# Performance work log

Measured on AMD Instinct MI355X. Metric: run time of the kernel, lower is better.

The kernel has to match this reference:

```python
import jax, jax.numpy as jnp
import numpy as np

V, C, T, H, L, B = 32000, 1024, 1024, 16, 8, 4
HS = C // H
STD = 0.02


def _layernorm(x, g, b, eps=1e-5):
    m = jnp.mean(x, axis=-1, keepdims=True)
    v = jnp.mean(jnp.square(x - m), axis=-1, keepdims=True)
    return (x - m) * jax.lax.rsqrt(v + eps) * g + b


def setup_inputs() -> dict:
    key = jax.random.key(0)
    ks = jax.random.split(key, 16)
    n = lambda k, shape: (jax.random.normal(k, shape, dtype=jnp.float32) * STD)
    return {
        "index": jax.random.randint(ks[0], (B, T), 0, V),
        "targets": jax.random.randint(ks[1], (B, T), 0, V),
        "tok_emb": n(ks[2], (V, C)),
        "pos_emb": n(ks[3], (T, C)),
        "wq": n(ks[4], (L, C, C)),
        "wk": n(ks[5], (L, C, C)),
        "wv": n(ks[6], (L, C, C)),
        "wo": n(ks[7], (L, C, C)),
        "bo": jnp.zeros((L, C), jnp.float32),
        "w1": n(ks[8], (L, C, 4 * C)),
        "b1": jnp.zeros((L, 4 * C), jnp.float32),
        "w2": n(ks[9], (L, 4 * C, C)),
        "b2": jnp.zeros((L, C), jnp.float32),
        "ln1_g": jnp.ones((L, C), jnp.float32),
        "ln1_b": jnp.zeros((L, C), jnp.float32),
        "ln2_g": jnp.ones((L, C), jnp.float32),
        "ln2_b": jnp.zeros((L, C), jnp.float32),
        "lnf_g": jnp.ones((C,), jnp.float32),
        "lnf_b": jnp.zeros((C,), jnp.float32),
        "lm_w": n(ks[10], (C, V)),
        "lm_b": jnp.zeros((V,), jnp.float32),
    }


def reference(index, targets, tok_emb, pos_emb, wq, wk, wv, wo, bo, w1, b1, w2,
              b2, ln1_g, ln1_b, ln2_g, ln2_b, lnf_g, lnf_b, lm_w, lm_b):
    b, t = index.shape
    x = tok_emb[index] + pos_emb[:t]                      # [B,T,C]
    causal = jnp.tril(jnp.ones((t, t), dtype=bool))       # tril mask
    scale = HS ** -0.5
    for l in range(L):  # fixed small layer loop
        q = (x @ wq[l]).reshape(b, t, H, HS)
        k = (x @ wk[l]).reshape(b, t, H, HS)
        v = (x @ wv[l]).reshape(b, t, H, HS)
        scores = jnp.einsum('bqhd,bkhd->bhqk', q, k) * scale
        scores = jnp.where(causal, scores, -jnp.inf)
        w = jax.nn.softmax(scores, axis=-1)               # dropout p=0 -> identity
        att = jnp.einsum('bhqk,bkhd->bqhd', w, v).reshape(b, t, C)
        x = _layernorm(x + att @ wo[l] + bo[l], ln1_g[l], ln1_b[l])
        h = jax.nn.relu(x @ w1[l] + b1[l])
        x = _layernorm(x + h @ w2[l] + b2[l], ln2_g[l], ln2_b[l])
    x = _layernorm(x, lnf_g, lnf_b)
    logits = (x @ lm_w + lm_b).reshape(b * t, V)
    logp = jax.nn.log_softmax(logits, axis=-1)
    loss = -jnp.take_along_axis(logp, targets.reshape(-1, 1), axis=1).mean()
    return logits, loss
```

## Files before the change

### kernel.cpp

```cpp
#include <hip/hip_runtime.h>

typedef unsigned short u16;
typedef __attribute__((ext_vector_type(4))) float f32x4;
typedef __attribute__((ext_vector_type(8))) short s16x8;

static constexpr int V = 32000;
static constexpr int C = 1024;
static constexpr int T = 1024;
static constexpr int H = 16;
static constexpr int L = 8;
static constexpr int B = 4;
static constexpr int HS = 64;
static constexpr int BT = B * T;
static constexpr int C4 = 4 * C;
static constexpr int C3 = 3 * C;

__device__ __forceinline__ u16 f2bf(float f) {
  union { float f; unsigned u; } v; v.f = f;
  unsigned r = v.u + 0x7fffu + ((v.u >> 16) & 1u);
  return (u16)(r >> 16);
}

__device__ __forceinline__ void gload16(const u16* g, u16* l) {
  __builtin_amdgcn_global_load_lds(
      (const __attribute__((address_space(1))) void*)g,
      (__attribute__((address_space(3))) void*)l, 16, 0, 0);
}

__device__ __forceinline__ float blockReduceSum(float v) {
  __shared__ float red[4];
  int lane = threadIdx.x & 63, w = threadIdx.x >> 6;
#pragma unroll
  for (int m = 32; m >= 1; m >>= 1) v += __shfl_xor(v, m, 64);
  if (lane == 0) red[w] = v;
  __syncthreads();
  float r = red[0] + red[1] + red[2] + red[3];
  __syncthreads();
  return r;
}

__global__ __launch_bounds__(256) void k_embed(
    const int* __restrict__ idx, const float* __restrict__ tok,
    const float* __restrict__ pos, float* __restrict__ x, u16* __restrict__ xb) {
  int bt = blockIdx.x;
  int t = bt & (T - 1);
  int row = idx[bt];
  const float* te = tok + (size_t)row * C;
  const float* pe = pos + (size_t)t * C;
  float* xo = x + (size_t)bt * C;
  u16* xbo = xb + (size_t)bt * C;
  for (int c = threadIdx.x; c < C; c += 256) {
    float v = te[c] + pe[c];
    xo[c] = v;
    xbo[c] = f2bf(v);
  }
}

__global__ __launch_bounds__(256) void k_transpose(
    const float* __restrict__ W, u16* __restrict__ Wt, int K, int N,
    size_t sW, size_t sWt) {
  __shared__ float tile[64][65];
  const float* Wz = W + sW * blockIdx.z;
  u16* Wtz = Wt + sWt * blockIdx.z;
  int n0 = blockIdx.x * 64, k0 = blockIdx.y * 64;
  int tc = threadIdx.x & 63, tr = threadIdx.x >> 6;
#pragma unroll
  for (int i = 0; i < 16; ++i) {
    int r = tr + i * 4;
    tile[r][tc] = Wz[(size_t)(k0 + r) * N + (n0 + tc)];
  }
  __syncthreads();
#pragma unroll
  for (int i = 0; i < 16; ++i) {
    int r = tr + i * 4;
    Wtz[(size_t)(n0 + r) * K + (k0 + tc)] = f2bf(tile[tc][r]);
  }
}

__global__ __launch_bounds__(256) void k_vtrans(
    const u16* __restrict__ qkv, u16* __restrict__ vt) {
  __shared__ u16 tile[64][72];
  int bid = blockIdx.x;
  int tc = bid & 15, h = (bid >> 4) & 15, b = bid >> 8;
  int t0 = tc * 64;
  const size_t base = (size_t)b * T * C3 + 2 * C + (size_t)h * HS;
  int tid = threadIdx.x;
  int r = tid >> 3, c8 = (tid & 7) * 8;
#pragma unroll
  for (int it = 0; it < 2; ++it) {
    int row = r + it * 32;
    *(s16x8*)&tile[row][c8] =
        *(const s16x8*)&qkv[base + (size_t)(t0 + row) * C3 + c8];
  }
  __syncthreads();
  const size_t vbase = (size_t)(b * H + h) * HS * T + t0;
#pragma unroll
  for (int it = 0; it < 2; ++it) {
    int d = (tid >> 3) + it * 32;
    s16x8 o;
#pragma unroll
    for (int j = 0; j < 8; ++j) o[j] = (short)tile[c8 + j][d];
    *(s16x8*)&vt[vbase + (size_t)d * T + c8] = o;
  }
}

template <int OUT_BF16, int RELU, int HAS_BIAS, int HAS_RES>
__global__ __launch_bounds__(256, 2) void k_gemm(
    const u16* __restrict__ A, const u16* __restrict__ Bt,
    const float* __restrict__ bias, const float* __restrict__ Res,
    float* __restrict__ Cf, u16* __restrict__ Cb, int M, int N, int K) {
  __shared__ u16 As[128 * 32];
  __shared__ u16 Bs[128 * 32];
  int tid = threadIdx.x;
  int lane = tid & 63, wid = tid >> 6;
  int lm = lane & 15, lg = lane >> 4;
  int wm = wid >> 1, wn = wid & 1;

  unsigned nbx = gridDim.x;
  unsigned nwg = nbx * gridDim.y;
  unsigned orig = blockIdx.y * nbx + blockIdx.x;
  unsigned f = ((nwg & 7u) == 0u) ? (orig & 7u) * (nwg >> 3) + (orig >> 3) : orig;
  int mb = (int)(f / nbx) * 128, nb = (int)(f % nbx) * 128;

  f32x4 acc[4][4];
#pragma unroll
  for (int i = 0; i < 4; ++i)
#pragma unroll
    for (int j = 0; j < 4; ++j) acc[i][j] = f32x4{0.f, 0.f, 0.f, 0.f};

  int r0 = tid >> 2, q0 = tid & 3;
  int r1 = (256 + tid) >> 2, q1 = tid & 3;
  const u16* a0 = A + (size_t)(mb + r0) * K + q0 * 8;
  const u16* a1 = A + (size_t)(mb + r1) * K + q1 * 8;
  const u16* b0 = Bt + (size_t)(nb + r0) * K + q0 * 8;
  const u16* b1 = Bt + (size_t)(nb + r1) * K + q1 * 8;
  u16* lA0 = &As[wid * 512];
  u16* lA1 = &As[2048 + wid * 512];
  u16* lB0 = &Bs[wid * 512];
  u16* lB1 = &Bs[2048 + wid * 512];

  int nK = K >> 5;
  for (int kb = 0; kb < nK; ++kb) {
    __syncthreads();
    int ko = kb * 32;
    gload16(a0 + ko, lA0);
    gload16(a1 + ko, lA1);
    gload16(b0 + ko, lB0);
    gload16(b1 + ko, lB1);
    __syncthreads();
    s16x8 af[4], bfr[4];
#pragma unroll
    for (int m = 0; m < 4; ++m)
      af[m] = *(const s16x8*)&As[(wm * 64 + m * 16 + lm) * 32 + lg * 8];
#pragma unroll
    for (int n = 0; n < 4; ++n)
      bfr[n] = *(const s16x8*)&Bs[(wn * 64 + n * 16 + lm) * 32 + lg * 8];
#pragma unroll
    for (int m = 0; m < 4; ++m)
#pragma unroll
      for (int n = 0; n < 4; ++n)
        acc[m][n] = __builtin_amdgcn_mfma_f32_16x16x32_bf16(af[m], bfr[n],
                                                            acc[m][n], 0, 0, 0);
  }
#pragma unroll
  for (int m = 0; m < 4; ++m) {
#pragma unroll
    for (int n = 0; n < 4; ++n) {
      int col = nb + wn * 64 + n * 16 + lm;
      float bv = HAS_BIAS ? bias[col] : 0.0f;
#pragma unroll
      for (int r = 0; r < 4; ++r) {
        int row = mb + wm * 64 + m * 16 + lg * 4 + r;
        float v = acc[m][n][r] + bv;
        if (HAS_RES) v += Res[(size_t)row * N + col];
        if (RELU) v = v > 0.f ? v : 0.f;
        if (OUT_BF16)
          Cb[(size_t)row * N + col] = f2bf(v);
        else
          Cf[(size_t)row * N + col] = v;
      }
    }
  }
}

template <int OUT_BF16, int RELU, int HAS_BIAS, int HAS_RES>
__global__ __launch_bounds__(512) void k_gemm256(
    const u16* __restrict__ A, const u16* __restrict__ Bt,
    const float* __restrict__ bias, const float* __restrict__ Res,
    float* __restrict__ Cf, u16* __restrict__ Cb, int M, int N, int K) {
  __shared__ u16 As[2][16384];
  __shared__ u16 Bs[2][16384];
  const int tid = threadIdx.x;
  const int lane = tid & 63, wid = tid >> 6;
  const int lm = lane & 15, lg = lane >> 4;
  const int wr = wid >> 2, wc = wid & 3;

  unsigned nbx = gridDim.x;
  unsigned nwg = nbx * gridDim.y;
  unsigned orig = blockIdx.y * nbx + blockIdx.x;
  unsigned f = ((nwg & 7u) == 0u) ? (orig & 7u) * (nwg >> 3) + (orig >> 3) : orig;
  const int mb = (int)(f / nbx) * 256, nb = (int)(f % nbx) * 256;

  int aoff[4], boff[4], ldso[4];
#pragma unroll
  for (int h = 0; h < 4; ++h) {
    const int kk = h >> 1, p = h & 1;
    int rem = p * 512 + tid;
    int rblk = rem >> 6;
    int rem2 = rem & 63;
    int row16 = rem2 >> 2, psl = rem2 & 3;
    int sl = psl ^ ((row16 >> 1) & 3);
    int grow = rblk * 16 + row16;
    int gk = kk * 32 + sl * 8;
    aoff[h] = (mb + grow) * K + gk;
    boff[h] = (nb + grow) * K + gk;
    ldso[h] = kk * 8192 + p * 4096 + wid * 512;
  }
  const int lo = lm * 32 + ((lg ^ ((lm >> 1) & 3)) << 3);

  f32x4 acc[8][4];
#pragma unroll
  for (int i = 0; i < 8; ++i)
#pragma unroll
    for (int j = 0; j < 4; ++j) acc[i][j] = f32x4{0.f, 0.f, 0.f, 0.f};

  const int nK = K >> 6;
  gload16(A + aoff[0], &As[0][ldso[0]]);
  gload16(A + aoff[1], &As[0][ldso[1]]);
  gload16(Bt + boff[0], &Bs[0][ldso[0]]);
  gload16(Bt + boff[1], &Bs[0][ldso[1]]);
  gload16(A + aoff[2], &As[0][ldso[2]]);
  gload16(A + aoff[3], &As[0][ldso[3]]);
  gload16(Bt + boff[2], &Bs[0][ldso[2]]);
  gload16(Bt + boff[3], &Bs[0][ldso[3]]);
  asm volatile("s_waitcnt vmcnt(4)" ::: "memory");
  __builtin_amdgcn_s_barrier();

  for (int t = 0; t < nK; ++t) {
    const int buf = t & 1, nbuf = buf ^ 1;
    const bool pre = (t + 1 < nK);
    const int nk64 = (t + 1) * 64;
    s16x8 af[4], bfr[4];
#pragma unroll
    for (int m = 0; m < 4; ++m)
      af[m] = *(const s16x8*)&As[buf][(wr * 8 + m) * 512 + lo];
#pragma unroll
    for (int n = 0; n < 4; ++n)
      bfr[n] = *(const s16x8*)&Bs[buf][(wc * 4 + n) * 512 + lo];
    if (pre) {
      gload16(A + aoff[0] + nk64, &As[nbuf][ldso[0]]);
      gload16(A + aoff[1] + nk64, &As[nbuf][ldso[1]]);
    }
    __builtin_amdgcn_s_barrier();
    __builtin_amdgcn_s_setprio(1);
#pragma unroll
    for (int m = 0; m < 4; ++m)
#pragma unroll
      for (int n = 0; n < 4; ++n)
        acc[m][n] = __builtin_amdgcn_mfma_f32_16x16x32_bf16(af[m], bfr[n],
                                                            acc[m][n], 0, 0, 0);
    __builtin_amdgcn_s_setprio(0);
    __builtin_amdgcn_s_barrier();
#pragma unroll
    for (int m = 0; m < 4; ++m)
      af[m] = *(const s16x8*)&As[buf][(wr * 8 + 4 + m) * 512 + lo];
    if (pre) {
      gload16(Bt + boff[0] + nk64, &Bs[nbuf][ldso[0]]);
      gload16(Bt + boff[1] + nk64, &Bs[nbuf][ldso[1]]);
    }
    __builtin_amdgcn_s_barrier();
    __builtin_amdgcn_s_setprio(1);
#pragma unroll
    for (int m = 0; m < 4; ++m)
#pragma unroll
      for (int n = 0; n < 4; ++n)
        acc[m + 4][n] = __builtin_amdgcn_mfma_f32_16x16x32_bf16(
            af[m], bfr[n], acc[m + 4][n], 0, 0, 0);
    __builtin_amdgcn_s_setprio(0);
    __builtin_amdgcn_s_barrier();
#pragma unroll
    for (int m = 0; m < 4; ++m)
      af[m] = *(const s16x8*)&As[buf][8192 + (wr * 8 + m) * 512 + lo];
#pragma unroll
    for (int n = 0; n < 4; ++n)
      bfr[n] = *(const s16x8*)&Bs[buf][8192 + (wc * 4 + n) * 512 + lo];
    if (pre) {
      gload16(A + aoff[2] + nk64, &As[nbuf][ldso[2]]);
      gload16(A + aoff[3] + nk64, &As[nbuf][ldso[3]]);
      asm volatile("s_waitcnt vmcnt(6)" ::: "memory");
    } else {
      asm volatile("s_waitcnt vmcnt(0)" ::: "memory");
    }
    __builtin_amdgcn_s_barrier();
    __builtin_amdgcn_s_setprio(1);
#pragma unroll
    for (int m = 0; m < 4; ++m)
#pragma unroll
      for (int n = 0; n < 4; ++n)
        acc[m][n] = __builtin_amdgcn_mfma_f32_16x16x32_bf16(af[m], bfr[n],
                                                            acc[m][n], 0, 0, 0);
    __builtin_amdgcn_s_setprio(0);
    __builtin_amdgcn_s_barrier();
#pragma unroll
    for (int m = 0; m < 4; ++m)
      af[m] = *(const s16x8*)&As[buf][8192 + (wr * 8 + 4 + m) * 512 + lo];
    if (pre) {
      gload16(Bt + boff[2] + nk64, &Bs[nbuf][ldso[2]]);
      gload16(Bt + boff[3] + nk64, &Bs[nbuf][ldso[3]]);
      asm volatile("s_waitcnt vmcnt(4)" ::: "memory");
    }
    __builtin_amdgcn_s_barrier();
    __builtin_amdgcn_s_setprio(1);
#pragma unroll
    for (int m = 0; m < 4; ++m)
#pragma unroll
      for (int n = 0; n < 4; ++n)
        acc[m + 4][n] = __builtin_amdgcn_mfma_f32_16x16x32_bf16(
            af[m], bfr[n], acc[m + 4][n], 0, 0, 0);
    __builtin_amdgcn_s_setprio(0);
    __builtin_amdgcn_s_barrier();
  }
  float bv[4];
#pragma unroll
  for (int n = 0; n < 4; ++n)
    bv[n] = HAS_BIAS ? bias[nb + wc * 64 + n * 16 + lm] : 0.0f;
#pragma unroll
  for (int m = 0; m < 8; ++m) {
#pragma unroll
    for (int r = 0; r < 4; ++r) {
      int row = mb + wr * 128 + m * 16 + lg * 4 + r;
#pragma unroll
      for (int n = 0; n < 4; ++n) {
        int col = nb + wc * 64 + n * 16 + lm;
        float v = acc[m][n][r] + bv[n];
        if (HAS_RES) v += Res[(size_t)row * N + col];
        if (RELU) v = v > 0.f ? v : 0.f;
        if (OUT_BF16)
          Cb[(size_t)row * N + col] = f2bf(v);
        else
          Cf[(size_t)row * N + col] = v;
      }
    }
  }
}

__global__ __launch_bounds__(256) void k_attn(
    const u16* __restrict__ qkv, const u16* __restrict__ vt,
    u16* __restrict__ o) {
  constexpr int PP = 72;
  __shared__ u16 Ks[64 * 64];
  __shared__ u16 Vs[64 * 64];
  __shared__ u16 Ps[4][16 * PP];
  int bid = blockIdx.x;
  int qt = bid & 15, h = (bid >> 4) & 15, b = bid >> 8;
  int tid = threadIdx.x, lane = tid & 63, wid = tid >> 6;
  int lm = lane & 15, lg = lane >> 4;
  const size_t rowbase = (size_t)b * T * C3 + (size_t)h * HS;
  const u16* kbase = qkv + rowbase + C;
  const u16* vbase = vt + (size_t)(b * H + h) * HS * T;
  int qb = qt * 64;
  int qw = qb + wid * 16;
  const float scale = 0.125f;

  s16x8 qf[2];
#pragma unroll
  for (int s = 0; s < 2; ++s)
    qf[s] = *(const s16x8*)&qkv[rowbase + (size_t)(qw + lm) * C3 + s * 32 + lg * 8];

  float m_[4], l_[4];
  f32x4 oacc[4];
#pragma unroll
  for (int r = 0; r < 4; ++r) { m_[r] = -3e38f; l_[r] = 0.f; }
#pragma unroll
  for (int n = 0; n < 4; ++n) oacc[n] = f32x4{0.f, 0.f, 0.f, 0.f};

  const int sr = tid >> 3, scs = (tid & 7) ^ (sr & 7);
  const int swz0 = ((lg) ^ (lm & 7)) * 8;
  const int swz1 = ((4 + lg) ^ (lm & 7)) * 8;

  for (int kt = 0; kt <= qt; ++kt) {
    __syncthreads();
    gload16(kbase + (size_t)(kt * 64 + sr) * C3 + scs * 8, &Ks[wid * 512]);
    gload16(kbase + (size_t)(kt * 64 + sr + 32) * C3 + scs * 8,
            &Ks[2048 + wid * 512]);
    gload16(vbase + (size_t)sr * T + kt * 64 + scs * 8, &Vs[wid * 512]);
    gload16(vbase + (size_t)(sr + 32) * T + kt * 64 + scs * 8,
            &Vs[2048 + wid * 512]);
    __syncthreads();

    f32x4 s[4];
#pragma unroll
    for (int ch = 0; ch < 4; ++ch) s[ch] = f32x4{0.f, 0.f, 0.f, 0.f};
#pragma unroll
    for (int ch = 0; ch < 4; ++ch) {
      s16x8 k0 = *(const s16x8*)&Ks[(ch * 16 + lm) * 64 + swz0];
      s16x8 k1 = *(const s16x8*)&Ks[(ch * 16 + lm) * 64 + swz1];
      s[ch] = __builtin_amdgcn_mfma_f32_16x16x32_bf16(qf[0], k0, s[ch], 0, 0, 0);
      s[ch] = __builtin_amdgcn_mfma_f32_16x16x32_bf16(qf[1], k1, s[ch], 0, 0, 0);
    }
    if (kt == qt) {
#pragma unroll
      for (int ch = 0; ch < 4; ++ch) {
        int col = kt * 64 + ch * 16 + lm;
#pragma unroll
        for (int r = 0; r < 4; ++r) {
          int row = qw + lg * 4 + r;
          s[ch][r] = (col <= row) ? s[ch][r] * scale : -3e38f;
        }
      }
    } else {
#pragma unroll
      for (int ch = 0; ch < 4; ++ch)
#pragma unroll
        for (int r = 0; r < 4; ++r) s[ch][r] *= scale;
    }
    float rmax[4];
#pragma unroll
    for (int r = 0; r < 4; ++r)
      rmax[r] = fmaxf(fmaxf(s[0][r], s[1][r]), fmaxf(s[2][r], s[3][r]));
#pragma unroll
    for (int mm = 1; mm < 16; mm <<= 1)
#pragma unroll
      for (int r = 0; r < 4; ++r)
        rmax[r] = fmaxf(rmax[r], __shfl_xor(rmax[r], mm, 16));
    float alpha[4], rsum[4];
#pragma unroll
    for (int r = 0; r < 4; ++r) {
      float mn = fmaxf(m_[r], rmax[r]);
      alpha[r] = __expf(m_[r] - mn);
      m_[r] = mn;
      rsum[r] = 0.f;
    }
#pragma unroll
    for (int ch = 0; ch < 4; ++ch)
#pragma unroll
      for (int r = 0; r < 4; ++r) {
        float e = __expf(s[ch][r] - m_[r]);
        s[ch][r] = e;
        rsum[r] += e;
      }
#pragma unroll
    for (int mm = 1; mm < 16; mm <<= 1)
#pragma unroll
      for (int r = 0; r < 4; ++r) rsum[r] += __shfl_xor(rsum[r], mm, 16);
#pragma unroll
    for (int r = 0; r < 4; ++r) l_[r] = l_[r] * alpha[r] + rsum[r];
#pragma unroll
    for (int n = 0; n < 4; ++n)
#pragma unroll
      for (int r = 0; r < 4; ++r) oacc[n][r] *= alpha[r];
#pragma unroll
    for (int r = 0; r < 4; ++r) {
      int pr = lg * 4 + r;
#pragma unroll
      for (int ch = 0; ch < 4; ++ch)
        Ps[wid][pr * PP + ch * 16 + lm] = f2bf(s[ch][r]);
    }
    s16x8 pa0 = *(const s16x8*)&Ps[wid][lm * PP + lg * 8];
    s16x8 pa1 = *(const s16x8*)&Ps[wid][lm * PP + 32 + lg * 8];
#pragma unroll
    for (int n = 0; n < 4; ++n) {
      s16x8 v0 = *(const s16x8*)&Vs[(n * 16 + lm) * 64 + swz0];
      s16x8 v1 = *(const s16x8*)&Vs[(n * 16 + lm) * 64 + swz1];
      oacc[n] = __builtin_amdgcn_mfma_f32_16x16x32_bf16(pa0, v0, oacc[n], 0, 0, 0);
      oacc[n] = __builtin_amdgcn_mfma_f32_16x16x32_bf16(pa1, v1, oacc[n], 0, 0, 0);
    }
  }
  const size_t obase = (size_t)b * T * C + (size_t)h * HS;
  float inv[4];
#pragma unroll
  for (int r = 0; r < 4; ++r) inv[r] = 1.0f / l_[r];
#pragma unroll
  for (int n = 0; n < 4; ++n)
#pragma unroll
    for (int r = 0; r < 4; ++r)
      o[obase + (size_t)(qw + lg * 4 + r) * C + n * 16 + lm] =
          f2bf(oacc[n][r] * inv[r]);
}

__global__ __launch_bounds__(256) void k_ln(
    const float* __restrict__ in, const float* __restrict__ g,
    const float* __restrict__ bsh, float* __restrict__ xout,
    u16* __restrict__ xbout) {
  int row = blockIdx.x;
  const float* xr = in + (size_t)row * C;
  int tid = threadIdx.x;
  float vals[4];
  float s = 0.f;
#pragma unroll
  for (int i = 0; i < 4; ++i) {
    float vv = xr[tid + i * 256];
    vals[i] = vv;
    s += vv;
  }
  s = blockReduceSum(s);
  float mean = s * (1.0f / C);
  float s2 = 0.f;
#pragma unroll
  for (int i = 0; i < 4; ++i) {
    float d = vals[i] - mean;
    s2 += d * d;
  }
  s2 = blockReduceSum(s2);
  float rstd = rsqrtf(s2 * (1.0f / C) + 1e-5f);
#pragma unroll
  for (int i = 0; i < 4; ++i) {
    int c = tid + i * 256;
    float y = (vals[i] - mean) * rstd * g[c] + bsh[c];
    xout[(size_t)row * C + c] = y;
    xbout[(size_t)row * C + c] = f2bf(y);
  }
}

__global__ __launch_bounds__(256) void k_rowloss(
    const float* __restrict__ logits, const int* __restrict__ tgt,
    float* __restrict__ rowloss) {
  int row = blockIdx.x;
  const float* lr = logits + (size_t)row * V;
  const f32x4* lr4 = (const f32x4*)lr;
  int tid = threadIdx.x;
  float m = -3e38f, s = 0.f;
  for (int i = tid; i < V / 4; i += 256) {
    f32x4 v = lr4[i];
#pragma unroll
    for (int j = 0; j < 4; ++j) {
      float x = v[j];
      if (x > m) {
        s = s * __expf(m - x) + 1.f;
        m = x;
      } else {
        s += __expf(x - m);
      }
    }
  }
#pragma unroll
  for (int d = 1; d < 64; d <<= 1) {
    float mo = __shfl_xor(m, d, 64), so = __shfl_xor(s, d, 64);
    float mn = fmaxf(m, mo);
    s = s * __expf(m - mn) + so * __expf(mo - mn);
    m = mn;
  }
  __shared__ float sm[4], ss[4];
  int w = tid >> 6;
  if ((tid & 63) == 0) { sm[w] = m; ss[w] = s; }
  __syncthreads();
  if (tid == 0) {
    float M = fmaxf(fmaxf(sm[0], sm[1]), fmaxf(sm[2], sm[3]));
    float S = ss[0] * __expf(sm[0] - M) + ss[1] * __expf(sm[1] - M) +
              ss[2] * __expf(sm[2] - M) + ss[3] * __expf(sm[3] - M);
    rowloss[row] = (M + logf(S)) - lr[tgt[row]];
  }
}

__global__ __launch_bounds__(256) void k_lossreduce(
    const float* __restrict__ rowloss, float* __restrict__ out) {
  __shared__ float red[256];
  int tid = threadIdx.x;
  float s = 0.f;
  for (int i = tid; i < BT; i += 256) s += rowloss[i];
  red[tid] = s;
  __syncthreads();
  for (int m = 128; m >= 1; m >>= 1) {
    if (tid < m) red[tid] += red[tid + m];
    __syncthreads();
  }
  if (tid == 0) out[0] = red[0] * (1.0f / BT);
}

extern "C" void kernel_launch(void* const* d_in, const int* in_sizes, int n_in,
                              void* d_out, int out_size, void* d_ws,
                              size_t ws_size, hipStream_t stream) {
  (void)in_sizes; (void)n_in; (void)out_size; (void)ws_size;
  const int* index = (const int*)d_in[0];
  const int* targets = (const int*)d_in[1];
  const float* tok_emb = (const float*)d_in[2];
  const float* pos_emb = (const float*)d_in[3];
  const float* wq = (const float*)d_in[4];
  const float* wk = (const float*)d_in[5];
  const float* wv = (const float*)d_in[6];
  const float* wo = (const float*)d_in[7];
  const float* bo = (const float*)d_in[8];
  const float* w1 = (const float*)d_in[9];
  const float* b1 = (const float*)d_in[10];
  const float* w2 = (const float*)d_in[11];
  const float* b2 = (const float*)d_in[12];
  const float* ln1_g = (const float*)d_in[13];
  const float* ln1_b = (const float*)d_in[14];
  const float* ln2_g = (const float*)d_in[15];
  const float* ln2_b = (const float*)d_in[16];
  const float* lnf_g = (const float*)d_in[17];
  const float* lnf_b = (const float*)d_in[18];
  const float* lm_w = (const float*)d_in[19];
  const float* lm_b = (const float*)d_in[20];

  float* logits = (float*)d_out;
  float* loss = logits + (size_t)BT * V;

  size_t off = 0;
  auto alloc = [&](size_t bytes) -> void* {
    off = (off + 255) & ~(size_t)255;
    void* p = (void*)((char*)d_ws + off);
    off += bytes;
    return p;
  };
  u16* wqkv_t = (u16*)alloc((size_t)L * C3 * C * 2);
  u16* wo_t = (u16*)alloc((size_t)L * C * C * 2);
  u16* w1_t = (u16*)alloc((size_t)L * C * C4 * 2);
  u16* w2_t = (u16*)alloc((size_t)L * C4 * C * 2);
  u16* lmw_t = (u16*)alloc((size_t)V * C * 2);
  float* x = (float*)alloc((size_t)BT * C * 4);
  float* tmp = (float*)alloc((size_t)BT * C * 4);
  u16* xb = (u16*)alloc((size_t)BT * C * 2);
  u16* qkvb = (u16*)alloc((size_t)BT * C3 * 2);
  u16* vtb = (u16*)alloc((size_t)BT * C * 2);
  u16* attb = (u16*)alloc((size_t)BT * C * 2);
  u16* hb = (u16*)alloc((size_t)BT * C4 * 2);
  float* rowloss = (float*)alloc((size_t)BT * 4);

  dim3 blk(256);
  dim3 blk5(512);
  k_transpose<<<dim3(C / 64, C / 64, L), blk, 0, stream>>>(
      wq, wqkv_t, C, C, (size_t)C * C, (size_t)C3 * C);
  k_transpose<<<dim3(C / 64, C / 64, L), blk, 0, stream>>>(
      wk, wqkv_t + (size_t)C * C, C, C, (size_t)C * C, (size_t)C3 * C);
  k_transpose<<<dim3(C / 64, C / 64, L), blk, 0, stream>>>(
      wv, wqkv_t + (size_t)2 * C * C, C, C, (size_t)C * C, (size_t)C3 * C);
  k_transpose<<<dim3(C / 64, C / 64, L), blk, 0, stream>>>(
      wo, wo_t, C, C, (size_t)C * C, (size_t)C * C);
  k_transpose<<<dim3(C4 / 64, C / 64, L), blk, 0, stream>>>(
      w1, w1_t, C, C4, (size_t)C * C4, (size_t)C * C4);
  k_transpose<<<dim3(C / 64, C4 / 64, L), blk, 0, stream>>>(
      w2, w2_t, C4, C, (size_t)C4 * C, (size_t)C4 * C);
  k_transpose<<<dim3(V / 64, C / 64, 1), blk, 0, stream>>>(
      lm_w, lmw_t, C, V, 0, 0);

  k_embed<<<BT, blk, 0, stream>>>(index, tok_emb, pos_emb, x, xb);

  dim3 gQKV(C3 / 128, BT / 128);
  dim3 gCC(C / 128, BT / 128);
  dim3 gC4(C4 / 256, BT / 256);
  for (int l = 0; l < L; ++l) {
    const u16* wqkvt = wqkv_t + (size_t)l * C3 * C;
    const u16* wot = wo_t + (size_t)l * C * C;
    const u16* w1t = w1_t + (size_t)l * C * C4;
    const u16* w2t = w2_t + (size_t)l * C4 * C;

    k_gemm<1, 0, 0, 0><<<gQKV, blk, 0, stream>>>(
        xb, wqkvt, nullptr, nullptr, nullptr, qkvb, BT, C3, C);
    k_vtrans<<<B * H * (T / 64), blk, 0, stream>>>(qkvb, vtb);
    k_attn<<<B * H * (T / 64), blk, 0, stream>>>(qkvb, vtb, attb);
    k_gemm<0, 0, 1, 1><<<gCC, blk, 0, stream>>>(
        attb, wot, bo + (size_t)l * C, x, tmp, nullptr, BT, C, C);
    k_ln<<<BT, blk, 0, stream>>>(tmp, ln1_g + (size_t)l * C,
                                 ln1_b + (size_t)l * C, x, xb);
    k_gemm256<1, 1, 1, 0><<<gC4, blk5, 0, stream>>>(
        xb, w1t, b1 + (size_t)l * C4, nullptr, nullptr, hb, BT, C4, C);
    k_gemm<0, 0, 1, 1><<<gCC, blk, 0, stream>>>(
        hb, w2t, b2 + (size_t)l * C, x, tmp, nullptr, BT, C, C4);
    k_ln<<<BT, blk, 0, stream>>>(tmp, ln2_g + (size_t)l * C,
                                 ln2_b + (size_t)l * C, x, xb);
  }
  k_ln<<<BT, blk, 0, stream>>>(x, lnf_g, lnf_b, x, xb);
  k_gemm256<0, 0, 1, 0><<<dim3(V / 256, BT / 256), blk5, 0, stream>>>(
      xb, lmw_t, lm_b, nullptr, logits, nullptr, BT, V, C);
  k_rowloss<<<BT, blk, 0, stream>>>(logits, targets, rowloss);
  k_lossreduce<<<1, blk, 0, stream>>>(rowloss, loss);
}
```

Baseline: 2.947 ms.

## Fuse V transpose into QKV GEMM epilogue and enlarge attention query tiles

The QKV projection now runs on the 256x256 GEMM kernel, and its epilogue writes the V columns straight into the transposed vt layout, which removes the separate transpose kernel and its extra global-memory round trip. The attention kernel now gives each block 128 queries, two 16-row groups per wave, so every K/V tile loaded into LDS is reused by twice as many queries. The cost is more registers per wave and fewer attention blocks for the GPU to spread across its compute units.

```diff
diff --git a/kernel.cpp b/kernel.cpp
--- a/kernel.cpp
+++ b/kernel.cpp
@@ -3,6 +3,7 @@
 typedef unsigned short u16;
 typedef __attribute__((ext_vector_type(4))) float f32x4;
 typedef __attribute__((ext_vector_type(8))) short s16x8;
+typedef __attribute__((ext_vector_type(4))) short s16x4;
 
 static constexpr int V = 32000;
 static constexpr int C = 1024;
@@ -77,33 +78,6 @@
   }
 }
 
-__global__ __launch_bounds__(256) void k_vtrans(
-    const u16* __restrict__ qkv, u16* __restrict__ vt) {
-  __shared__ u16 tile[64][72];
-  int bid = blockIdx.x;
-  int tc = bid & 15, h = (bid >> 4) & 15, b = bid >> 8;
-  int t0 = tc * 64;
-  const size_t base = (size_t)b * T * C3 + 2 * C + (size_t)h * HS;
-  int tid = threadIdx.x;
-  int r = tid >> 3, c8 = (tid & 7) * 8;
-#pragma unroll
-  for (int it = 0; it < 2; ++it) {
-    int row = r + it * 32;
-    *(s16x8*)&tile[row][c8] =
-        *(const s16x8*)&qkv[base + (size_t)(t0 + row) * C3 + c8];
-  }
-  __syncthreads();
-  const size_t vbase = (size_t)(b * H + h) * HS * T + t0;
-#pragma unroll
-  for (int it = 0; it < 2; ++it) {
-    int d = (tid >> 3) + it * 32;
-    s16x8 o;
-#pragma unroll
-    for (int j = 0; j < 8; ++j) o[j] = (short)tile[c8 + j][d];
-    *(s16x8*)&vt[vbase + (size_t)d * T + c8] = o;
-  }
-}
-
 template <int OUT_BF16, int RELU, int HAS_BIAS, int HAS_RES>
 __global__ __launch_bounds__(256, 2) void k_gemm(
     const u16* __restrict__ A, const u16* __restrict__ Bt,
@@ -183,11 +157,12 @@
   }
 }
 
-template <int OUT_BF16, int RELU, int HAS_BIAS, int HAS_RES>
+template <int OUT_BF16, int RELU, int HAS_BIAS, int HAS_RES, int VT>
 __global__ __launch_bounds__(512) void k_gemm256(
     const u16* __restrict__ A, const u16* __restrict__ Bt,
     const float* __restrict__ bias, const float* __restrict__ Res,
-    float* __restrict__ Cf, u16* __restrict__ Cb, int M, int N, int K) {
+    float* __restrict__ Cf, u16* __restrict__ Cb, u16* __restrict__ Vtp,
+    int M, int N, int K) {
   __shared__ u16 As[2][16384];
   __shared__ u16 Bs[2][16384];
   const int tid = threadIdx.x;
@@ -320,6 +295,24 @@
     __builtin_amdgcn_s_setprio(0);
     __builtin_amdgcn_s_barrier();
   }
+  if (VT && nb >= 2 * C) {
+    int hh = ((nb - 2 * C) >> 6) + wc;
+#pragma unroll
+    for (int m = 0; m < 8; ++m) {
+      int t0 = mb + wr * 128 + m * 16 + lg * 4;
+      int bb = t0 >> 10, tt = t0 & (T - 1);
+      size_t vbase = ((size_t)(bb * H + hh) * HS) * T + tt;
+#pragma unroll
+      for (int n = 0; n < 4; ++n) {
+        int d = n * 16 + lm;
+        s16x4 pk;
+#pragma unroll
+        for (int r = 0; r < 4; ++r) pk[r] = (short)f2bf(acc[m][n][r]);
+        *(s16x4*)&Vtp[vbase + (size_t)d * T] = pk;
+      }
+    }
+    return;
+  }
   float bv[4];
 #pragma unroll
   for (int n = 0; n < 4; ++n)
@@ -350,35 +343,43 @@
   constexpr int PP = 72;
   __shared__ u16 Ks[64 * 64];
   __shared__ u16 Vs[64 * 64];
-  __shared__ u16 Ps[4][16 * PP];
+  __shared__ u16 Ps[4][32 * PP];
   int bid = blockIdx.x;
-  int qt = bid & 15, h = (bid >> 4) & 15, b = bid >> 8;
+  int qt = bid & 7, h = (bid >> 3) & 15, b = bid >> 7;
   int tid = threadIdx.x, lane = tid & 63, wid = tid >> 6;
   int lm = lane & 15, lg = lane >> 4;
   const size_t rowbase = (size_t)b * T * C3 + (size_t)h * HS;
   const u16* kbase = qkv + rowbase + C;
   const u16* vbase = vt + (size_t)(b * H + h) * HS * T;
-  int qb = qt * 64;
-  int qw = qb + wid * 16;
+  int qb = qt * 128;
+  int qw = qb + wid * 32;
   const float scale = 0.125f;
 
-  s16x8 qf[2];
-#pragma unroll
-  for (int s = 0; s < 2; ++s)
-    qf[s] = *(const s16x8*)&qkv[rowbase + (size_t)(qw + lm) * C3 + s * 32 + lg * 8];
-
-  float m_[4], l_[4];
-  f32x4 oacc[4];
-#pragma unroll
-  for (int r = 0; r < 4; ++r) { m_[r] = -3e38f; l_[r] = 0.f; }
-#pragma unroll
-  for (int n = 0; n < 4; ++n) oacc[n] = f32x4{0.f, 0.f, 0.f, 0.f};
-
+  s16x8 qf[2][2];
+#pragma unroll
+  for (int g = 0; g < 2; ++g)
+#pragma unroll
+    for (int s = 0; s < 2; ++s)
+      qf[g][s] = *(const s16x8*)&qkv[rowbase +
+          (size_t)(qw + g * 16 + lm) * C3 + s * 32 + lg * 8];
+
+  float m_[2][4], l_[2][4];
+  f32x4 oacc[2][4];
+#pragma unroll
+  for (int g = 0; g < 2; ++g)
+#pragma unroll
+    for (int r = 0; r < 4; ++r) { m_[g][r] = -3e38f; l_[g][r] = 0.f; }
+#pragma unroll
+  for (int g = 0; g < 2; ++g)
+#pragma unroll
+    for (int n = 0; n < 4; ++n) oacc[g][n] = f32x4{0.f, 0.f, 0.f, 0.f};
+
+  const int nkt = (qb + 128) >> 6;
   const int sr = tid >> 3, scs = (tid & 7) ^ (sr & 7);
-  const int swz0 = ((lg) ^ (lm & 7)) * 8;
+  const int swz0 = (lg ^ (lm & 7)) * 8;
   const int swz1 = ((4 + lg) ^ (lm & 7)) * 8;
 
-  for (int kt = 0; kt <= qt; ++kt) {
+  for (int kt = 0; kt < nkt; ++kt) {
     __syncthreads();
     gload16(kbase + (size_t)(kt * 64 + sr) * C3 + scs * 8, &Ks[wid * 512]);
     gload16(kbase + (size_t)(kt * 64 + sr + 32) * C3 + scs * 8,
@@ -388,94 +389,115 @@
             &Vs[2048 + wid * 512]);
     __syncthreads();
 
-    f32x4 s[4];
-#pragma unroll
-    for (int ch = 0; ch < 4; ++ch) s[ch] = f32x4{0.f, 0.f, 0.f, 0.f};
+    s16x8 k0[4], k1[4];
 #pragma unroll
     for (int ch = 0; ch < 4; ++ch) {
-      s16x8 k0 = *(const s16x8*)&Ks[(ch * 16 + lm) * 64 + swz0];
-      s16x8 k1 = *(const s16x8*)&Ks[(ch * 16 + lm) * 64 + swz1];
-      s[ch] = __builtin_amdgcn_mfma_f32_16x16x32_bf16(qf[0], k0, s[ch], 0, 0, 0);
-      s[ch] = __builtin_amdgcn_mfma_f32_16x16x32_bf16(qf[1], k1, s[ch], 0, 0, 0);
-    }
-    if (kt == qt) {
+      k0[ch] = *(const s16x8*)&Ks[(ch * 16 + lm) * 64 + swz0];
+      k1[ch] = *(const s16x8*)&Ks[(ch * 16 + lm) * 64 + swz1];
+    }
+#pragma unroll
+    for (int g = 0; g < 2; ++g) {
+      f32x4 s[4];
 #pragma unroll
       for (int ch = 0; ch < 4; ++ch) {
-        int col = kt * 64 + ch * 16 + lm;
+        s[ch] = f32x4{0.f, 0.f, 0.f, 0.f};
+        s[ch] = __builtin_amdgcn_mfma_f32_16x16x32_bf16(qf[g][0], k0[ch],
+                                                        s[ch], 0, 0, 0);
+        s[ch] = __builtin_amdgcn_mfma_f32_16x16x32_bf16(qf[g][1], k1[ch],
+                                                        s[ch], 0, 0, 0);
+      }
+      int grow = qw + g * 16;
+      if (kt * 64 + 63 > grow) {
+#pragma unroll
+        for (int ch = 0; ch < 4; ++ch) {
+          int col = kt * 64 + ch * 16 + lm;
+#pragma unroll
+          for (int r = 0; r < 4; ++r) {
+            int row = grow + lg * 4 + r;
+            s[ch][r] = (col <= row) ? s[ch][r] * scale : -3e38f;
+          }
+        }
+      } else {
+#pragma unroll
+        for (int ch = 0; ch < 4; ++ch)
+#pragma unroll
+          for (int r = 0; r < 4; ++r) s[ch][r] *= scale;
+      }
+      float rmax[4];
+#pragma unroll
+      for (int r = 0; r < 4; ++r)
+        rmax[r] = fmaxf(fmaxf(s[0][r], s[1][r]), fmaxf(s[2][r], s[3][r]));
+#pragma unroll
+      for (int mm = 1; mm < 16; mm <<= 1)
+#pragma unroll
+        for (int r = 0; r < 4; ++r)
+          rmax[r] = fmaxf(rmax[r], __shfl_xor(rmax[r], mm, 16));
+      float alpha[4], rsum[4];
+#pragma unroll
+      for (int r = 0; r < 4; ++r) {
+        float mn = fmaxf(m_[g][r], rmax[r]);
+        alpha[r] = __expf(m_[g][r] - mn);
+        m_[g][r] = mn;
+        rsum[r] = 0.f;
+      }
+#pragma unroll
+      for (int ch = 0; ch < 4; ++ch)
 #pragma unroll
         for (int r = 0; r < 4; ++r) {
-          int row = qw + lg * 4 + r;
-          s[ch][r] = (col <= row) ? s[ch][r] * scale : -3e38f;
+          float e = __expf(s[ch][r] - m_[g][r]);
+          s[ch][r] = e;
+          rsum[r] += e;
         }
-      }
-    } else {
-#pragma unroll
-      for (int ch = 0; ch < 4; ++ch)
-#pragma unroll
-        for (int r = 0; r < 4; ++r) s[ch][r] *= scale;
-    }
-    float rmax[4];
-#pragma unroll
-    for (int r = 0; r < 4; ++r)
-      rmax[r] = fmaxf(fmaxf(s[0][r], s[1][r]), fmaxf(s[2][r], s[3][r]));
-#pragma unroll
-    for (int mm = 1; mm < 16; mm <<= 1)
+#pragma unroll
+      for (int mm = 1; mm < 16; mm <<= 1)
+#pragma unroll
+        for (int r = 0; r < 4; ++r) rsum[r] += __shfl_xor(rsum[r], mm, 16);
+#pragma unroll
+      for (int r = 0; r < 4; ++r) l_[g][r] = l_[g][r] * alpha[r] + rsum[r];
+#pragma unroll
+      for (int n = 0; n < 4; ++n)
+#pragma unroll
+        for (int r = 0; r < 4; ++r) oacc[g][n][r] *= alpha[r];
+#pragma unroll
+      for (int r = 0; r < 4; ++r) {
+        int pr = g * 16 + lg * 4 + r;
+#pragma unroll
+        for (int ch = 0; ch < 4; ++ch)
+          Ps[wid][pr * PP + ch * 16 + lm] = f2bf(s[ch][r]);
+      }
+    }
+    s16x8 v0[4], v1[4];
+#pragma unroll
+    for (int n = 0; n < 4; ++n) {
+      v0[n] = *(const s16x8*)&Vs[(n * 16 + lm) * 64 + swz0];
+      v1[n] = *(const s16x8*)&Vs[(n * 16 + lm) * 64 + swz1];
+    }
+#pragma unroll
+    for (int g = 0; g < 2; ++g) {
+      s16x8 pa0 = *(const s16x8*)&Ps[wid][(g * 16 + lm) * PP + lg * 8];
+      s16x8 pa1 = *(const s16x8*)&Ps[wid][(g * 16 + lm) * PP + 32 + lg * 8];
+#pragma unroll
+      for (int n = 0; n < 4; ++n) {
+        oacc[g][n] = __builtin_amdgcn_mfma_f32_16x16x32_bf16(pa0, v0[n],
+                                                             oacc[g][n], 0, 0, 0);
+        oacc[g][n] = __builtin_amdgcn_mfma_f32_16x16x32_bf16(pa1, v1[n],
+                                                             oacc[g][n], 0, 0, 0);
+      }
+    }
+  }
+  const size_t obase = (size_t)b * T * C + (size_t)h * HS;
+#pragma unroll
+  for (int g = 0; g < 2; ++g) {
+    float inv[4];
+#pragma unroll
+    for (int r = 0; r < 4; ++r) inv[r] = 1.0f / l_[g][r];
+#pragma unroll
+    for (int n = 0; n < 4; ++n)
 #pragma unroll
       for (int r = 0; r < 4; ++r)
-        rmax[r] = fmaxf(rmax[r], __shfl_xor(rmax[r], mm, 16));
-    float alpha[4], rsum[4];
-#pragma unroll
-    for (int r = 0; r < 4; ++r) {
-      float mn = fmaxf(m_[r], rmax[r]);
-      alpha[r] = __expf(m_[r] - mn);
-      m_[r] = mn;
-      rsum[r] = 0.f;
-    }
-#pragma unroll
-    for (int ch = 0; ch < 4; ++ch)
-#pragma unroll
-      for (int r = 0; r < 4; ++r) {
-        float e = __expf(s[ch][r] - m_[r]);
-        s[ch][r] = e;
-        rsum[r] += e;
-      }
-#pragma unroll
-    for (int mm = 1; mm < 16; mm <<= 1)
-#pragma unroll
-      for (int r = 0; r < 4; ++r) rsum[r] += __shfl_xor(rsum[r], mm, 16);
-#pragma unroll
-    for (int r = 0; r < 4; ++r) l_[r] = l_[r] * alpha[r] + rsum[r];
-#pragma unroll
-    for (int n = 0; n < 4; ++n)
-#pragma unroll
-      for (int r = 0; r < 4; ++r) oacc[n][r] *= alpha[r];
-#pragma unroll
-    for (int r = 0; r < 4; ++r) {
-      int pr = lg * 4 + r;
-#pragma unroll
-      for (int ch = 0; ch < 4; ++ch)
-        Ps[wid][pr * PP + ch * 16 + lm] = f2bf(s[ch][r]);
-    }
-    s16x8 pa0 = *(const s16x8*)&Ps[wid][lm * PP + lg * 8];
-    s16x8 pa1 = *(const s16x8*)&Ps[wid][lm * PP + 32 + lg * 8];
-#pragma unroll
-    for (int n = 0; n < 4; ++n) {
-      s16x8 v0 = *(const s16x8*)&Vs[(n * 16 + lm) * 64 + swz0];
-      s16x8 v1 = *(const s16x8*)&Vs[(n * 16 + lm) * 64 + swz1];
-      oacc[n] = __builtin_amdgcn_mfma_f32_16x16x32_bf16(pa0, v0, oacc[n], 0, 0, 0);
-      oacc[n] = __builtin_amdgcn_mfma_f32_16x16x32_bf16(pa1, v1, oacc[n], 0, 0, 0);
-    }
-  }
-  const size_t obase = (size_t)b * T * C + (size_t)h * HS;
-  float inv[4];
-#pragma unroll
-  for (int r = 0; r < 4; ++r) inv[r] = 1.0f / l_[r];
-#pragma unroll
-  for (int n = 0; n < 4; ++n)
-#pragma unroll
-    for (int r = 0; r < 4; ++r)
-      o[obase + (size_t)(qw + lg * 4 + r) * C + n * 16 + lm] =
-          f2bf(oacc[n][r] * inv[r]);
+        o[obase + (size_t)(qw + g * 16 + lg * 4 + r) * C + n * 16 + lm] =
+            f2bf(oacc[g][n][r] * inv[r]);
+  }
 }
 
 __global__ __launch_bounds__(256) void k_ln(
@@ -636,7 +658,7 @@
 
   k_embed<<<BT, blk, 0, stream>>>(index, tok_emb, pos_emb, x, xb);
 
-  dim3 gQKV(C3 / 128, BT / 128);
+  dim3 gQKV(C3 / 256, BT / 256);
   dim3 gCC(C / 128, BT / 128);
   dim3 gC4(C4 / 256, BT / 256);
   for (int l = 0; l < L; ++l) {
@@ -645,24 +667,23 @@
     const u16* w1t = w1_t + (size_t)l * C * C4;
     const u16* w2t = w2_t + (size_t)l * C4 * C;
 
-    k_gemm<1, 0, 0, 0><<<gQKV, blk, 0, stream>>>(
-        xb, wqkvt, nullptr, nullptr, nullptr, qkvb, BT, C3, C);
-    k_vtrans<<<B * H * (T / 64), blk, 0, stream>>>(qkvb, vtb);
-    k_attn<<<B * H * (T / 64), blk, 0, stream>>>(qkvb, vtb, attb);
+    k_gemm256<1, 0, 0, 0, 1><<<gQKV, blk5, 0, stream>>>(
+        xb, wqkvt, nullptr, nullptr, nullptr, qkvb, vtb, BT, C3, C);
+    k_attn<<<B * H * (T / 128), blk, 0, stream>>>(qkvb, vtb, attb);
     k_gemm<0, 0, 1, 1><<<gCC, blk, 0, stream>>>(
         attb, wot, bo + (size_t)l * C, x, tmp, nullptr, BT, C, C);
     k_ln<<<BT, blk, 0, stream>>>(tmp, ln1_g + (size_t)l * C,
                                  ln1_b + (size_t)l * C, x, xb);
-    k_gemm256<1, 1, 1, 0><<<gC4, blk5, 0, stream>>>(
-        xb, w1t, b1 + (size_t)l * C4, nullptr, nullptr, hb, BT, C4, C);
+    k_gemm256<1, 1, 1, 0, 0><<<gC4, blk5, 0, stream>>>(
+        xb, w1t, b1 + (size_t)l * C4, nullptr, nullptr, hb, nullptr, BT, C4, C);
     k_gemm<0, 0, 1, 1><<<gCC, blk, 0, stream>>>(
         hb, w2t, b2 + (size_t)l * C, x, tmp, nullptr, BT, C, C4);
     k_ln<<<BT, blk, 0, stream>>>(tmp, ln2_g + (size_t)l * C,
                                  ln2_b + (size_t)l * C, x, xb);
   }
   k_ln<<<BT, blk, 0, stream>>>(x, lnf_g, lnf_b, x, xb);
-  k_gemm256<0, 0, 1, 0><<<dim3(V / 256, BT / 256), blk5, 0, stream>>>(
-      xb, lmw_t, lm_b, nullptr, logits, nullptr, BT, V, C);
+  k_gemm256<0, 0, 1, 0, 0><<<dim3(V / 256, BT / 256), blk5, 0, stream>>>(
+      xb, lmw_t, lm_b, nullptr, logits, nullptr, nullptr, BT, V, C);
   k_rowloss<<<BT, blk, 0, stream>>>(logits, targets, rowloss);
   k_lossreduce<<<1, blk, 0, stream>>>(rowloss, loss);
 }
```

New measurement: 2.891 ms. Within noise of the previous version (-1.9%).
